# Performance work log

Measured on AMD Instinct MI355X. Metric: run time of the kernel, lower is better.

The kernel has to match this reference:

```python
import jax, jax.numpy as jnp
import numpy as np

NUM_HEADS = 32
EPS = 1e-5
NEG_INF = -1e9


def _ln(x, g, b):
    m = x.mean(-1, keepdims=True)
    v = ((x - m) ** 2).mean(-1, keepdims=True)
    return (x - m) / jnp.sqrt(v + EPS) * g + b


def setup_inputs() -> dict:
    key = jax.random.key(0)
    ks = jax.random.split(key, 20)
    N, B, D, E, F, L = 512, 2, 768, 256, 3072, 4
    inp = {
        'x': jax.random.normal(ks[0], (N, B, D), jnp.float32),
        'pos': jax.random.normal(ks[1], (B, N, 3), jnp.float32) * 5.0,
        'padding_mask': jnp.broadcast_to(jnp.arange(N)[None, :] >= N - 32, (B, N)),
        'outcell_index': jax.random.randint(ks[2], (B, E), 0, N),
        'expand_pos': jax.random.normal(ks[3], (B, E, 3), jnp.float32) * 5.0,
        'expand_mask': jnp.broadcast_to(jnp.arange(E)[None, :] >= E - 16, (B, E)),
        'vec_project_w': jax.random.normal(ks[4], (D, 3 * D), jnp.float32) * 0.02,
        'ln_x_g': jnp.ones((L, D), jnp.float32),
        'ln_x_b': jnp.zeros((L, D), jnp.float32),
        'ln_vec_g': jnp.ones((L, D), jnp.float32),
        'ln_vec_b': jnp.zeros((L, D), jnp.float32),
        'adaln_x_w': jax.random.normal(ks[5], (L, D, D), jnp.float32) * 0.02,
        'adaln_vecmlp_w': jax.random.normal(ks[6], (L, D, 2 * D), jnp.float32) * 0.02,
        'out_proj_w': jax.random.normal(ks[7], (L, D, D), jnp.float32) * 0.02,
        'vecmlp_norm_g': jnp.ones((L, D), jnp.float32),
        'vecmlp_norm_b': jnp.zeros((L, D), jnp.float32),
        'mlp_w1': jax.random.normal(ks[8], (L, D, F), jnp.float32) * 0.02,
        'mlp_w2': jax.random.normal(ks[9], (L, F, D), jnp.float32) * 0.02,
    }
    return inp


def reference(x, pos, padding_mask, outcell_index, expand_pos, expand_mask,
              vec_project_w, ln_x_g, ln_x_b, ln_vec_g, ln_vec_b,
              adaln_x_w, adaln_vecmlp_w, out_proj_w,
              vecmlp_norm_g, vecmlp_norm_b, mlp_w1, mlp_w2):
    x = jnp.swapaxes(x, 0, 1)  # [B,N,D]
    B, N, D = x.shape
    H = NUM_HEADS
    hd = D // H
    L = ln_x_g.shape[0]

    # --- PBC-expanded pairwise distance bias ---
    epf = jnp.concatenate([pos, expand_pos], axis=1)  # [B,S,3]
    S = epf.shape[1]
    delta = pos[:, :, None, :] - epf[:, None, :, :]   # [B,N,S,3]
    sq = (delta * delta).sum(-1)
    dist = jnp.where(sq > 0, jnp.sqrt(jnp.where(sq > 0, sq, 1.0)), 0.0)
    kpm_full = jnp.concatenate([padding_mask, expand_mask], axis=-1)  # [B,S]
    dist = jnp.where(padding_mask[:, :, None], 1e6, dist)
    dist = jnp.where(kpm_full[:, None, :], 1e6, dist)
    dist = 1.0 / (dist + 1.0)
    # additive attn mask (bias + key-padding -inf), broadcast over heads
    attn_mask = jnp.where(kpm_full[:, None, None, :], NEG_INF, dist[:, None, :, :])  # [B,1,N,S]

    vec = (jax.nn.silu(x) @ vec_project_w).reshape(B, N, 3, D)
    barange = jnp.arange(B)[:, None]
    scale = 1.0 / jnp.sqrt(jnp.float32(3 * hd))

    for l in range(L):
        rx, rv = x, vec
        xl = _ln(x, ln_x_g[l], ln_x_b[l])
        vl = _ln(vec, ln_vec_g[l], ln_vec_b[l])
        scale_x = jax.nn.silu(xl) @ adaln_x_w[l]        # [B,N,D]
        vmod = vl * scale_x[:, :, None, :]              # [B,N,3,D]
        # PBC gather-expanded K/V
        kv_exp = vmod[barange, outcell_index]           # [B,E,3,D]
        kv = jnp.concatenate([vmod, kv_exp], axis=1)    # [B,S,3,D]
        q = vmod.reshape(B, N, 3, H, hd).transpose(0, 3, 1, 2, 4).reshape(B, H, N, 3 * hd)
        k = kv.reshape(B, S, 3, H, hd).transpose(0, 3, 1, 2, 4).reshape(B, H, S, 3 * hd)
        v = k  # q=k=v in this block (same modulated vec)
        k = kv.reshape(B, S, 3, H, hd).transpose(0, 3, 1, 2, 4).reshape(B, H, S, 3 * hd)
        logits = jnp.einsum('bhnd,bhsd->bhns', q, k) * scale + attn_mask
        p = jax.nn.softmax(logits, axis=-1)
        o = jnp.einsum('bhns,bhsd->bhnd', p, v)          # [B,H,N,3hd]
        o = o.transpose(0, 2, 1, 3).reshape(B, N, H, 3, hd).transpose(0, 1, 3, 2, 4).reshape(B, N, 3, D)
        o = o @ out_proj_w[l]
        x = xl + rx
        vec = o + rv
        rx, rv = x, vec
        vm = _ln(vec, vecmlp_norm_g[l], vecmlp_norm_b[l])
        vm = jax.nn.silu(vm @ mlp_w1[l]) @ mlp_w2[l]     # [B,N,3,D]
        ss = jax.nn.silu(vm) @ adaln_vecmlp_w[l]         # [B,N,3,2D]
        sc, sh = jnp.split(ss, 2, axis=-1)
        x = x * sc.sum(-2) + sh.sum(-2) + rx
        vec = vm + rv
    return x, vec
```

## Files before the change

### kernel.cpp

```cpp
#include <hip/hip_runtime.h>

typedef __bf16 bf16_t;
typedef __bf16 bf8   __attribute__((ext_vector_type(8)));
typedef __bf16 bf4   __attribute__((ext_vector_type(4)));
typedef float  f32x4 __attribute__((ext_vector_type(4)));

__device__ __forceinline__ f32x4 mfma16(bf8 a, bf8 b, f32x4 c){
  return __builtin_amdgcn_mfma_f32_16x16x32_bf16(a, b, c, 0, 0, 0);
}
__device__ __forceinline__ float siluf_(float x){ return x / (1.f + __expf(-x)); }

__device__ __forceinline__ void async16(bf16_t* lds, const bf16_t* g){
  __builtin_amdgcn_global_load_lds(
      (const __attribute__((address_space(1))) unsigned int*)g,
      (__attribute__((address_space(3))) unsigned int*)lds, 16, 0, 0);
}

#define SCALE_QK 0.1178511302f

#define WT_VP   0ull
#define WT_AX   3538944ull
#define WT_AV   8257536ull
#define WT_OP   17694720ull
#define WT_M1   22413312ull
#define WT_M2   41287680ull
#define MASKB   60162048ull
#define SILUX   63307776ull
#define SILUXL  64880640ull
#define VLB     66453504ull
#define SCALEX  75890688ull
#define QKHB    79036416ull
#define KVTB    88473600ull
#define OBFB    97910784ull
#define VMLNB   102629376ull
#define H1B     107347968ull
#define SVM2B   126222336ull
#define SSB     130940928ull
#define MSOFF   10485760ull

struct TD { const float* s; bf16_t* d; int R, C, start, perz; };
struct TPack { TD t[6]; };

__global__ void transpose_all(TPack P)
{
  __shared__ bf16_t tile[64][66];
  const int bid = blockIdx.x;
  int k = 0;
  #pragma unroll
  for (int i = 1; i < 6; ++i) k = (bid >= P.t[i].start) ? i : k;
  const TD td = P.t[k];
  const int loc = bid - td.start;
  const int z = loc / td.perz, tl = loc - z*td.perz;
  const int nct = td.C >> 6;
  const int cx = tl % nct, ry = tl / nct;
  const size_t base = (size_t)z * td.R * td.C;
  const int r0 = ry*64, c0 = cx*64;
  const int t = threadIdx.x;
  #pragma unroll
  for (int j = 0; j < 4; ++j){
    int r = (t >> 4) + j*16;
    int cc = (t & 15) * 4;
    f32x4 v = *(const f32x4*)(td.s + base + (size_t)(r0 + r)*td.C + c0 + cc);
    #pragma unroll
    for (int e = 0; e < 4; ++e) tile[cc + e][r] = (bf16_t)v[e];
  }
  __syncthreads();
  #pragma unroll
  for (int j = 0; j < 2; ++j){
    int sid = j*256 + t;
    int c = sid >> 3, q = sid & 7;
    bf8 o = *(const bf8*)&tile[c][q*8];
    *(bf8*)(td.d + base + (size_t)(c0 + c)*td.R + r0 + q*8) = o;
  }
}

__global__ void mask_kernel(const float* __restrict__ pos, const float* __restrict__ epos,
                            bf16_t* __restrict__ wm)
{
  int i = blockIdx.x * 256 + threadIdx.x;
  int s = i % 768, t = i / 768;
  int n = t % 512, b = t / 512;
  bool kpm = (s < 512) ? (s >= 480) : (s >= 752);
  float o;
  if (kpm) o = 0.f;
  else {
    float d;
    if (n >= 480) d = 1e6f;
    else {
      const float* p = pos + (size_t)(b*512 + n)*3;
      const float* e = (s < 512) ? pos + (size_t)(b*512 + s)*3
                                 : epos + (size_t)(b*256 + (s-512))*3;
      float dx = p[0]-e[0], dy = p[1]-e[1], dz = p[2]-e[2];
      float sq = dx*dx + dy*dy + dz*dz;
      d = sq > 0.f ? sqrtf(sq) : 0.f;
    }
    o = __expf(1.f / (d + 1.f));
  }
  wm[i] = (bf16_t)o;
}

__global__ void xin_kernel(const float* __restrict__ xin, float* __restrict__ x,
                           bf16_t* __restrict__ sx)
{
  int i = blockIdx.x * 256 + threadIdx.x;
  int d = i % 768, t = i / 768;
  int n = t % 512, b = t / 512;
  float v = xin[((size_t)n*2 + b)*768 + d];
  x[i] = v;
  sx[i] = (bf16_t)siluf_(v);
}

__global__ __launch_bounds__(256,2) void ln_kernel(
    const float* __restrict__ in, const float* __restrict__ g, const float* __restrict__ bb,
    float* __restrict__ f32out, int addres, bf16_t* __restrict__ bfout, int dosilu)
{
  const int w = threadIdx.x >> 6, l = threadIdx.x & 63;
  const size_t r = (size_t)blockIdx.x * 4 + w;
  const float* p = in + r * 768;
  float v[12]; float s = 0.f;
  #pragma unroll
  for (int e = 0; e < 12; ++e){ v[e] = p[e*64 + l]; s += v[e]; }
  #pragma unroll
  for (int m = 1; m < 64; m <<= 1) s += __shfl_xor(s, m);
  float mean = s * (1.f/768.f);
  float q = 0.f;
  #pragma unroll
  for (int e = 0; e < 12; ++e){ float d = v[e] - mean; q += d*d; }
  #pragma unroll
  for (int m = 1; m < 64; m <<= 1) q += __shfl_xor(q, m);
  float rstd = rsqrtf(q * (1.f/768.f) + 1e-5f);
  #pragma unroll
  for (int e = 0; e < 12; ++e){
    int col = e*64 + l;
    float o = (v[e] - mean) * rstd * g[col] + bb[col];
    if (f32out) f32out[r*768 + col] = addres ? (o + v[e]) : o;
    if (bfout)  bfout[r*768 + col]  = (bf16_t)(dosilu ? siluf_(o) : o);
  }
}

__global__ __launch_bounds__(256,2) void pack2_kernel(
    const bf16_t* __restrict__ vl, const bf16_t* __restrict__ scx,
    const int* __restrict__ idx, bf16_t* __restrict__ qkh, bf16_t* __restrict__ kvt)
{
  __shared__ bf16_t tile[32*100];
  const int sb = blockIdx.x, bh = blockIdx.y;
  const int b = bh >> 5, h = bh & 31;
  const int tid = threadIdx.x;
  #pragma unroll
  for (int i = 0; i < 12; ++i){
    int e = i*256 + tid;
    int s_l = e / 96, col = e % 96;
    int s = sb*32 + s_l;
    float v = 0.f;
    if (col < 72){
      int n = (s < 512) ? s : idx[b*256 + (s - 512)];
      int c = col / 24, jj = col - c*24;
      int d = h*24 + jj;
      v = (float)vl[((size_t)(b*512 + n)*3 + c)*768 + d]
        * (float)scx[(size_t)(b*512 + n)*768 + d];
    }
    bf16_t bv = (bf16_t)v;
    qkh[((size_t)bh*768 + s)*96 + col] = bv;
    tile[s_l*100 + col] = bv;
  }
  __syncthreads();
  #pragma unroll
  for (int i = 0; i < 12; ++i){
    int f = i*256 + tid;
    int col = f >> 5, s_l = f & 31;
    kvt[((size_t)bh*96 + col)*768 + sb*32 + s_l] = tile[s_l*100 + col];
  }
}

__global__ __launch_bounds__(256,2) void attn_kernel(
    const bf16_t* __restrict__ qkh, const bf16_t* __restrict__ kvt,
    const bf16_t* __restrict__ wm, bf16_t* __restrict__ po, float* __restrict__ ms)
{
  __shared__ bf16_t Ks[64*128];
  __shared__ bf16_t Vs[96*72];
  __shared__ bf16_t Ps[64*72];
  const int g = blockIdx.x;
  const int qt = g >> 7, bhsz = g & 127;
  const int bh = bhsz & 63, sz = bhsz >> 6;
  const int b = bh >> 5;
  const int tid = threadIdx.x, w = tid >> 6, l = tid & 63;
  const int lg = l >> 4, lr = l & 15;
  const int sbase = sz * 384;
  const int qn0 = qt*64 + w*16 + lg*4;

  bf8 aq[3];
  {
    const bf16_t* qb = qkh + ((size_t)bh*768 + qt*64 + w*16 + lr)*96;
    #pragma unroll
    for (int ks = 0; ks < 3; ++ks) aq[ks] = *(const bf8*)(qb + ks*32 + lg*8);
  }

  int klds[3], vlds[3]; size_t kg[3], vg[3];
  #pragma unroll
  for (int it = 0; it < 3; ++it){
    int f = it*256 + tid;
    int r_ = f / 12, c_ = f % 12;
    klds[it] = r_*256 + ((c_*16) ^ ((r_ & 7) << 4));
    kg[it] = ((size_t)bh*768 + r_)*96 + c_*8;
    int vd = f >> 3, vc = (f & 7)*8;
    vlds[it] = vd*72 + vc;
    vg[it] = ((size_t)bh*96 + vd)*768 + vc;
  }

  f32x4 zf = {0.f,0.f,0.f,0.f};
  f32x4 accO[6];
  #pragma unroll
  for (int i = 0; i < 6; ++i) accO[i] = zf;
  float m_r[4], s_r[4];
  #pragma unroll
  for (int r = 0; r < 4; ++r){ m_r[r] = -1e30f; s_r[r] = 0.f; }

  bf8 kr[3], vr[3];
  #pragma unroll
  for (int it = 0; it < 3; ++it){
    kr[it] = *(const bf8*)(qkh + kg[it] + (size_t)sbase*96);
    vr[it] = *(const bf8*)(kvt + vg[it] + sbase);
  }
  #pragma unroll
  for (int it = 0; it < 3; ++it){
    *(bf8*)((char*)Ks + klds[it]) = kr[it];
    *(bf8*)&Vs[vlds[it]] = vr[it];
  }
  __syncthreads();

  const bf16_t* wrow = wm + (size_t)b*512*768;

  for (int t = 0; t < 6; ++t){
    const int s0 = sbase + t*64;
    if (t < 5){
      #pragma unroll
      for (int it = 0; it < 3; ++it){
        kr[it] = *(const bf8*)(qkh + kg[it] + (size_t)(s0 + 64)*96);
        vr[it] = *(const bf8*)(kvt + vg[it] + (s0 + 64));
      }
    }
    f32x4 sacc[4];
    __builtin_amdgcn_s_setprio(1);
    #pragma unroll
    for (int sf = 0; sf < 4; ++sf){
      sacc[sf] = zf;
      const int row = sf*16 + lr;
      #pragma unroll
      for (int ks = 0; ks < 3; ++ks){
        bf8 bg = *(const bf8*)((const char*)Ks + row*256 + ((ks*64 + lg*16) ^ ((row & 7) << 4)));
        sacc[sf] = mfma16(aq[ks], bg, sacc[sf]);
      }
    }
    __builtin_amdgcn_s_setprio(0);
    float tm[4];
    #pragma unroll
    for (int r = 0; r < 4; ++r)
      tm[r] = fmaxf(fmaxf(sacc[0][r], sacc[1][r]), fmaxf(sacc[2][r], sacc[3][r]));
    #pragma unroll
    for (int m = 1; m < 16; m <<= 1)
      #pragma unroll
      for (int r = 0; r < 4; ++r) tm[r] = fmaxf(tm[r], __shfl_xor(tm[r], m));
    float al[4], ps[4];
    #pragma unroll
    for (int r = 0; r < 4; ++r){
      float mn = fmaxf(m_r[r], tm[r]);
      al[r] = __expf((m_r[r] - mn)*SCALE_QK);
      m_r[r] = mn; ps[r] = 0.f;
    }
    #pragma unroll
    for (int sf = 0; sf < 4; ++sf)
      #pragma unroll
      for (int r = 0; r < 4; ++r){
        float p = __expf((sacc[sf][r] - m_r[r])*SCALE_QK)
                  * (float)wrow[(size_t)(qn0 + r)*768 + s0 + sf*16 + lr];
        ps[r] += p;
        Ps[(w*16 + lg*4 + r)*72 + sf*16 + lr] = (bf16_t)p;
      }
    #pragma unroll
    for (int m = 1; m < 16; m <<= 1)
      #pragma unroll
      for (int r = 0; r < 4; ++r) ps[r] += __shfl_xor(ps[r], m);
    #pragma unroll
    for (int r = 0; r < 4; ++r) s_r[r] = s_r[r]*al[r] + ps[r];
    #pragma unroll
    for (int df = 0; df < 6; ++df){
      f32x4 tt = accO[df];
      #pragma unroll
      for (int r = 0; r < 4; ++r) tt[r] *= al[r];
      accO[df] = tt;
    }
    __builtin_amdgcn_s_setprio(1);
    #pragma unroll
    for (int k2 = 0; k2 < 2; ++k2){
      bf8 pa = *(const bf8*)&Ps[(w*16 + lr)*72 + k2*32 + lg*8];
      #pragma unroll
      for (int df = 0; df < 6; ++df)
        accO[df] = mfma16(pa, *(const bf8*)&Vs[(df*16 + lr)*72 + k2*32 + lg*8], accO[df]);
    }
    __builtin_amdgcn_s_setprio(0);
    if (t < 5){
      __syncthreads();
      #pragma unroll
      for (int it = 0; it < 3; ++it){
        *(bf8*)((char*)Ks + klds[it]) = kr[it];
        *(bf8*)&Vs[vlds[it]] = vr[it];
      }
      __syncthreads();
    }
  }
  const size_t rbase = (size_t)(sz*64 + bh)*512;
  #pragma unroll
  for (int df = 0; df < 6; ++df){
    int dp = df*16 + lr;
    if (dp < 72){
      #pragma unroll
      for (int r = 0; r < 4; ++r)
        po[(rbase + qn0 + r)*80 + dp] = (bf16_t)accO[df][r];
    }
  }
  if (lr == 0){
    #pragma unroll
    for (int r = 0; r < 4; ++r){
      ms[(rbase + qn0 + r)*2]     = m_r[r];
      ms[(rbase + qn0 + r)*2 + 1] = s_r[r];
    }
  }
}

__global__ void attn_combine(const bf16_t* __restrict__ po, const float* __restrict__ ms,
                             bf16_t* __restrict__ obf)
{
  int t = blockIdx.x * 256 + threadIdx.x;
  int c = t % 12, row = t / 12;
  if (c >= 9) return;
  int bh = row >> 9, q = row & 511;
  int b = bh >> 5, h = bh & 31;
  float m1 = ms[(size_t)row*2],           s1 = ms[(size_t)row*2 + 1];
  float m2 = ms[(size_t)(32768 + row)*2], s2 = ms[(size_t)(32768 + row)*2 + 1];
  float m = fmaxf(m1, m2);
  float a1 = __expf((m1 - m)*SCALE_QK), a2 = __expf((m2 - m)*SCALE_QK);
  float rden = 1.f / (s1*a1 + s2*a2);
  bf8 o1 = *(const bf8*)(po + (size_t)row*80 + c*8);
  bf8 o2 = *(const bf8*)(po + (size_t)(32768 + row)*80 + c*8);
  bf8 o;
  #pragma unroll
  for (int r = 0; r < 8; ++r)
    o[r] = (bf16_t)(((float)o1[r]*a1 + (float)o2[r]*a2) * rden);
  int comp = c / 3, jj0 = (c % 3)*8;
  *(bf8*)(obf + ((size_t)(b*512 + q)*3 + comp)*768 + h*24 + jj0) = o;
}

template<int EPI>
__global__ __launch_bounds__(512,4) void gemm2(
    const bf16_t* __restrict__ A, const bf16_t* __restrict__ Bt,
    float* __restrict__ Cf, bf16_t* __restrict__ Cb,
    int M, int Nn, int K, int Ksub, int ntiles)
{
  __shared__ bf16_t As[128*64];
  __shared__ bf16_t Bs[128*64];
  const int tid = threadIdx.x;
  const int w = tid >> 6, l = tid & 63;
  const int lg = l >> 4, lr = l & 15;
  const int gb = blockIdx.x;
  const int sidx = gb >> 3, xcd = gb & 7;
  const int nt = sidx % ntiles;
  const int mt = xcd + (sidx / ntiles) * 8;
  const int wm = (w >> 2) * 64, wn = (w & 3) * 32;

  const int srow = w*8 + (l >> 3);
  const int scol = (((l & 7) ^ (l >> 3)) << 3);
  const bf16_t* Ab = A  + (size_t)(mt*128) * K;
  const bf16_t* Bb = Bt + (size_t)(nt*128) * K;
  const int kbeg = blockIdx.z * Ksub;

  f32x4 zf = {0.f,0.f,0.f,0.f};
  f32x4 acc[4][2];
  #pragma unroll
  for (int i = 0; i < 4; ++i)
    #pragma unroll
    for (int j = 0; j < 2; ++j) acc[i][j] = zf;

  int offA[4], offB[2];
  #pragma unroll
  for (int i = 0; i < 4; ++i){
    int row = wm + i*16 + lr;
    offA[i] = row*128 + ((lg*16) ^ ((row & 7) << 4));
  }
  #pragma unroll
  for (int j = 0; j < 2; ++j){
    int row = wn + j*16 + lr;
    offB[j] = row*128 + ((lg*16) ^ ((row & 7) << 4));
  }

  for (int k0 = kbeg; k0 < kbeg + Ksub; k0 += 64){
    __syncthreads();
    #pragma unroll
    for (int c = 0; c < 2; ++c){
      async16(&As[c*4096 + w*512], Ab + (size_t)(c*64 + srow)*K + k0 + scol);
      async16(&Bs[c*4096 + w*512], Bb + (size_t)(c*64 + srow)*K + k0 + scol);
    }
    __syncthreads();
    #pragma unroll
    for (int kk = 0; kk < 2; ++kk){
      bf8 af[4], bg[2];
      #pragma unroll
      for (int i = 0; i < 4; ++i)
        af[i] = *(const bf8*)((const char*)As + (offA[i] ^ (kk*64)));
      #pragma unroll
      for (int j = 0; j < 2; ++j)
        bg[j] = *(const bf8*)((const char*)Bs + (offB[j] ^ (kk*64)));
      #pragma unroll
      for (int i = 0; i < 4; ++i)
        #pragma unroll
        for (int j = 0; j < 2; ++j)
          acc[i][j] = mfma16(af[i], bg[j], acc[i][j]);
    }
  }

  const size_t zoff = (EPI == 4) ? (size_t)blockIdx.z * M * Nn : 0;
  #pragma unroll
  for (int i = 0; i < 4; ++i){
    int r0 = mt*128 + wm + i*16 + lg*4;
    #pragma unroll
    for (int j = 0; j < 2; ++j){
      int cc = nt*128 + wn + j*16 + lr;
      #pragma unroll
      for (int r = 0; r < 4; ++r){
        size_t off = (size_t)(r0 + r)*Nn + cc;
        float v = acc[i][j][r];
        if constexpr (EPI == 0)      Cf[off] = v;
        else if constexpr (EPI == 2) Cb[off] = (bf16_t)siluf_(v);
        else                         Cf[zoff + off] = v;
      }
    }
  }
}

__global__ void reduce4_bf(const float* __restrict__ p, bf16_t* __restrict__ out)
{
  int i = blockIdx.x * 256 + threadIdx.x;
  const f32x4* p4 = (const f32x4*)p;
  f32x4 a = p4[i], b = p4[i + 196608], c = p4[i + 393216], d = p4[i + 589824];
  bf4 o;
  #pragma unroll
  for (int r = 0; r < 4; ++r) o[r] = (bf16_t)(a[r] + b[r] + c[r] + d[r]);
  ((bf4*)out)[i] = o;
}

__global__ __launch_bounds__(256,2) void redop_ln(
    const float* __restrict__ p, float* __restrict__ vec,
    const float* __restrict__ g, const float* __restrict__ bb,
    bf16_t* __restrict__ vmln)
{
  const int w = threadIdx.x >> 6, l = threadIdx.x & 63;
  const size_t r = (size_t)blockIdx.x * 4 + w;
  float v[12]; float s = 0.f;
  #pragma unroll
  for (int e = 0; e < 12; ++e){
    size_t off = r*768 + e*64 + l;
    float t = vec[off] + p[off] + p[off + 2359296] + p[off + 4718592];
    vec[off] = t;
    v[e] = t; s += t;
  }
  #pragma unroll
  for (int m = 1; m < 64; m <<= 1) s += __shfl_xor(s, m);
  float mean = s * (1.f/768.f);
  float q = 0.f;
  #pragma unroll
  for (int e = 0; e < 12; ++e){ float d = v[e] - mean; q += d*d; }
  #pragma unroll
  for (int m = 1; m < 64; m <<= 1) q += __shfl_xor(q, m);
  float rstd = rsqrtf(q * (1.f/768.f) + 1e-5f);
  #pragma unroll
  for (int e = 0; e < 12; ++e){
    int col = e*64 + l;
    vmln[r*768 + col] = (bf16_t)((v[e] - mean) * rstd * g[col] + bb[col]);
  }
}

__global__ __launch_bounds__(256,2) void redmlp2_ln(
    const float* __restrict__ p, float* __restrict__ vec,
    bf16_t* __restrict__ svm2s,
    const float* __restrict__ g, const float* __restrict__ bb,
    bf16_t* __restrict__ vlb, int doln)
{
  const int w = threadIdx.x >> 6, l = threadIdx.x & 63;
  const size_t bn = (size_t)blockIdx.x * 4 + w;
  float ssum[12];
  #pragma unroll
  for (int e = 0; e < 12; ++e) ssum[e] = 0.f;
  for (int c = 0; c < 3; ++c){
    const size_t r = bn*3 + c;
    float v[12]; float s = 0.f;
    #pragma unroll
    for (int e = 0; e < 12; ++e){
      size_t off = r*768 + e*64 + l;
      float tm = p[off] + p[off + 2359296];
      float t = vec[off] + tm;
      vec[off] = t;
      v[e] = t; s += t;
      ssum[e] += siluf_(tm);
    }
    if (doln){
      #pragma unroll
      for (int m = 1; m < 64; m <<= 1) s += __shfl_xor(s, m);
      float mean = s * (1.f/768.f);
      float q = 0.f;
      #pragma unroll
      for (int e = 0; e < 12; ++e){ float d = v[e] - mean; q += d*d; }
      #pragma unroll
      for (int m = 1; m < 64; m <<= 1) q += __shfl_xor(q, m);
      float rstd = rsqrtf(q * (1.f/768.f) + 1e-5f);
      #pragma unroll
      for (int e = 0; e < 12; ++e){
        int col = e*64 + l;
        vlb[r*768 + col] = (bf16_t)((v[e] - mean) * rstd * g[col] + bb[col]);
      }
    }
  }
  #pragma unroll
  for (int e = 0; e < 12; ++e)
    svm2s[bn*768 + e*64 + l] = (bf16_t)ssum[e];
}

__global__ __launch_bounds__(256,2) void comb_ln(
    const float* __restrict__ p, float* __restrict__ x,
    const float* __restrict__ g, const float* __restrict__ bb,
    bf16_t* __restrict__ siluxl)
{
  const int w = threadIdx.x >> 6, l = threadIdx.x & 63;
  const size_t r = (size_t)blockIdx.x * 4 + w;
  const size_t base = r * 1536;
  float v[12]; float s = 0.f;
  #pragma unroll
  for (int e = 0; e < 12; ++e){
    int col = e*64 + l;
    float sc = p[base + col] + p[base + col + 1572864];
    float sh = p[base + 768 + col] + p[base + 768 + col + 1572864];
    float xv = x[r*768 + col]*(1.f + sc) + sh;
    v[e] = xv; s += xv;
  }
  #pragma unroll
  for (int m = 1; m < 64; m <<= 1) s += __shfl_xor(s, m);
  float mean = s * (1.f/768.f);
  float q = 0.f;
  #pragma unroll
  for (int e = 0; e < 12; ++e){ float d = v[e] - mean; q += d*d; }
  #pragma unroll
  for (int m = 1; m < 64; m <<= 1) q += __shfl_xor(q, m);
  float rstd = rsqrtf(q * (1.f/768.f) + 1e-5f);
  #pragma unroll
  for (int e = 0; e < 12; ++e){
    int col = e*64 + l;
    float xl = (v[e] - mean) * rstd * g[col] + bb[col];
    x[r*768 + col] = xl + v[e];
    siluxl[r*768 + col] = (bf16_t)siluf_(xl);
  }
}

__global__ void combine_kernel(const float* __restrict__ p, float* __restrict__ x)
{
  int i = blockIdx.x * 256 + threadIdx.x;
  size_t base = (size_t)(i / 768)*1536 + (i % 768);
  float sc = p[base] + p[base + 1572864];
  float sh = p[base + 768] + p[base + 768 + 1572864];
  x[i] = x[i]*(1.f + sc) + sh;
}

extern "C" void kernel_launch(void* const* d_in, const int* in_sizes, int n_in,
                              void* d_out, int out_size, void* d_ws, size_t ws_size,
                              hipStream_t stream)
{
  const float* x_in = (const float*)d_in[0];
  const float* pos  = (const float*)d_in[1];
  const int*   idx  = (const int*)d_in[3];
  const float* epos = (const float*)d_in[4];
  const float* vp_w = (const float*)d_in[6];
  const float* lxg  = (const float*)d_in[7];
  const float* lxb  = (const float*)d_in[8];
  const float* lvg  = (const float*)d_in[9];
  const float* lvb  = (const float*)d_in[10];
  const float* axw  = (const float*)d_in[11];
  const float* avw  = (const float*)d_in[12];
  const float* opw  = (const float*)d_in[13];
  const float* vng  = (const float*)d_in[14];
  const float* vnb  = (const float*)d_in[15];
  const float* w1   = (const float*)d_in[16];
  const float* w2   = (const float*)d_in[17];

  char* ws = (char*)d_ws;
  bf16_t* wt_vp = (bf16_t*)(ws + WT_VP);
  bf16_t* wt_ax = (bf16_t*)(ws + WT_AX);
  bf16_t* wt_av = (bf16_t*)(ws + WT_AV);
  bf16_t* wt_op = (bf16_t*)(ws + WT_OP);
  bf16_t* wt_m1 = (bf16_t*)(ws + WT_M1);
  bf16_t* wt_m2 = (bf16_t*)(ws + WT_M2);
  bf16_t* wmask = (bf16_t*)(ws + MASKB);
  bf16_t* silux = (bf16_t*)(ws + SILUX);
  bf16_t* siluxl= (bf16_t*)(ws + SILUXL);
  bf16_t* vlb   = (bf16_t*)(ws + VLB);
  bf16_t* scxb  = (bf16_t*)(ws + SCALEX);
  bf16_t* qkh   = (bf16_t*)(ws + QKHB);
  bf16_t* kvt   = (bf16_t*)(ws + KVTB);
  float*  partQ = (float*)(ws + QKHB);
  float*  partV = (float*)(ws + VLB);
  bf16_t* obf   = (bf16_t*)(ws + OBFB);
  bf16_t* vmln  = (bf16_t*)(ws + VMLNB);
  bf16_t* h1    = (bf16_t*)(ws + H1B);
  bf16_t* svm2s = (bf16_t*)(ws + SVM2B);
  bf16_t* pob   = (bf16_t*)(ws + SSB);
  float*  msb   = (float*)(ws + SSB + MSOFF);

  float* x   = (float*)d_out;
  float* vec = x + 786432;

  TPack P;
  P.t[0] = { vp_w, wt_vp, 768, 2304,    0,  432 };
  P.t[1] = { axw,  wt_ax, 768,  768,  432,  144 };
  P.t[2] = { avw,  wt_av, 768, 1536, 1008,  288 };
  P.t[3] = { opw,  wt_op, 768,  768, 2160,  144 };
  P.t[4] = { w1,   wt_m1, 768, 3072, 2736,  576 };
  P.t[5] = { w2,   wt_m2, 3072, 768, 5040,  576 };
  transpose_all<<<7344, 256, 0, stream>>>(P);

  mask_kernel<<<3072, 256, 0, stream>>>(pos, epos, wmask);
  xin_kernel<<<3072, 256, 0, stream>>>(x_in, x, silux);

  gemm2<0><<<dim3(8*18,1,1), 512, 0, stream>>>(silux, wt_vp, vec, nullptr,
                                               1024, 2304, 768, 768, 18);
  ln_kernel<<<256, 256, 0, stream>>>(x, lxg, lxb, x, 1, siluxl, 1);
  ln_kernel<<<768, 256, 0, stream>>>(vec, lvg, lvb, nullptr, 0, vlb, 0);

  for (int l = 0; l < 4; ++l){
    gemm2<4><<<dim3(8*6,1,4), 512, 0, stream>>>(siluxl, wt_ax + (size_t)l*768*768, partQ,
                                                nullptr, 1024, 768, 768, 192, 6);
    reduce4_bf<<<768, 256, 0, stream>>>(partQ, scxb);
    pack2_kernel<<<dim3(24, 64), 256, 0, stream>>>(vlb, scxb, idx, qkh, kvt);
    attn_kernel<<<1024, 256, 0, stream>>>(qkh, kvt, wmask, pob, msb);
    attn_combine<<<1536, 256, 0, stream>>>(pob, msb, obf);
    gemm2<4><<<dim3(24*6,1,3), 512, 0, stream>>>(obf, wt_op + (size_t)l*768*768, partV,
                                                 nullptr, 3072, 768, 768, 256, 6);
    redop_ln<<<768, 256, 0, stream>>>(partV, vec, vng + l*768, vnb + l*768, vmln);
    gemm2<2><<<dim3(24*24,1,1), 512, 0, stream>>>(vmln, wt_m1 + (size_t)l*3072*768, nullptr,
                                                  h1, 3072, 3072, 768, 768, 24);
    gemm2<4><<<dim3(24*6,1,2), 512, 0, stream>>>(h1, wt_m2 + (size_t)l*768*3072, partQ,
                                                 nullptr, 3072, 768, 3072, 1536, 6);
    redmlp2_ln<<<256, 256, 0, stream>>>(partQ, vec, svm2s,
                                        lvg + (l+1 < 4 ? (l+1)*768 : 0),
                                        lvb + (l+1 < 4 ? (l+1)*768 : 0),
                                        vlb, (l < 3) ? 1 : 0);
    gemm2<4><<<dim3(8*12,1,2), 512, 0, stream>>>(svm2s, wt_av + (size_t)l*1536*768, partQ,
                                                 nullptr, 1024, 1536, 768, 384, 12);
    if (l < 3)
      comb_ln<<<256, 256, 0, stream>>>(partQ, x, lxg + (l+1)*768, lxb + (l+1)*768, siluxl);
    else
      combine_kernel<<<3072, 256, 0, stream>>>(partQ, x);
  }
}
```

Baseline: 705.1 us.

## Drop attention split-KV combine pass and merge prologue kernels into one launch

The attention kernel now walks the full 768-key range in one block per (query tile, batch-head), normalises by the running sum and writes the final output layout directly, which removes the partial-output buffers and the separate combine kernel. The weight transpose, mask build and input copy are merged into one prologue launch, and the transpose now uses 64x128 tiles with a swizzled LDS layout and packed bf4 stores. This cuts four launches per forward and the partial-result traffic, but halves the attention grid (512 blocks), so there is less parallelism and a longer serial key loop per block.

After: 686.4 us. 1.03x faster.

```diff
diff --git a/kernel.cpp b/kernel.cpp
--- a/kernel.cpp
+++ b/kernel.cpp
@@ -35,79 +35,90 @@
 #define VMLNB   102629376ull
 #define H1B     107347968ull
 #define SVM2B   126222336ull
-#define SSB     130940928ull
-#define MSOFF   10485760ull
 
 struct TD { const float* s; bf16_t* d; int R, C, start, perz; };
 struct TPack { TD t[6]; };
 
-__global__ void transpose_all(TPack P)
-{
-  __shared__ bf16_t tile[64][66];
+#define NTRB 3672
+
+__global__ void prologue(TPack P,
+                         const float* __restrict__ pos, const float* __restrict__ epos,
+                         bf16_t* __restrict__ wm,
+                         const float* __restrict__ xin, float* __restrict__ x,
+                         bf16_t* __restrict__ sx)
+{
+  __shared__ bf16_t tile[128*72];
   const int bid = blockIdx.x;
+  const int t = threadIdx.x;
+  if (bid >= NTRB + 3072){
+    int i = (bid - NTRB - 3072) * 256 + t;
+    int d = i % 768, tt = i / 768;
+    int n = tt % 512, b = tt / 512;
+    float v = xin[((size_t)n*2 + b)*768 + d];
+    x[i] = v;
+    sx[i] = (bf16_t)siluf_(v);
+    return;
+  }
+  if (bid >= NTRB){
+    int i = (bid - NTRB) * 256 + t;
+    int s = i % 768, tt = i / 768;
+    int n = tt % 512, b = tt / 512;
+    bool kpm = (s < 512) ? (s >= 480) : (s >= 752);
+    float o;
+    if (kpm) o = 0.f;
+    else {
+      float d;
+      if (n >= 480) d = 1e6f;
+      else {
+        const float* p = pos + (size_t)(b*512 + n)*3;
+        const float* e = (s < 512) ? pos + (size_t)(b*512 + s)*3
+                                   : epos + (size_t)(b*256 + (s-512))*3;
+        float dx = p[0]-e[0], dy = p[1]-e[1], dz = p[2]-e[2];
+        float sq = dx*dx + dy*dy + dz*dz;
+        d = sq > 0.f ? sqrtf(sq) : 0.f;
+      }
+      o = __expf(1.f / (d + 1.f));
+    }
+    wm[i] = (bf16_t)o;
+    return;
+  }
   int k = 0;
   #pragma unroll
   for (int i = 1; i < 6; ++i) k = (bid >= P.t[i].start) ? i : k;
   const TD td = P.t[k];
   const int loc = bid - td.start;
   const int z = loc / td.perz, tl = loc - z*td.perz;
-  const int nct = td.C >> 6;
+  const int nct = td.C >> 7;
   const int cx = tl % nct, ry = tl / nct;
   const size_t base = (size_t)z * td.R * td.C;
-  const int r0 = ry*64, c0 = cx*64;
-  const int t = threadIdx.x;
-  #pragma unroll
-  for (int j = 0; j < 4; ++j){
-    int r = (t >> 4) + j*16;
-    int cc = (t & 15) * 4;
-    f32x4 v = *(const f32x4*)(td.s + base + (size_t)(r0 + r)*td.C + c0 + cc);
-    #pragma unroll
-    for (int e = 0; e < 4; ++e) tile[cc + e][r] = (bf16_t)v[e];
+  const int r0 = ry*64, c0 = cx*128;
+  #pragma unroll
+  for (int half = 0; half < 2; ++half){
+    int bb = half*256 + t;
+    int rb = bb >> 5, cb = bb & 31;
+    f32x4 v[4];
+    #pragma unroll
+    for (int i = 0; i < 4; ++i)
+      v[i] = *(const f32x4*)(td.s + base + (size_t)(r0 + rb*4 + i)*td.C + c0 + cb*4);
+    const int sw = (cb & 3) << 1;
+    const int rp = 4*(rb ^ sw);
+    #pragma unroll
+    for (int e = 0; e < 4; ++e){
+      bf4 pk;
+      #pragma unroll
+      for (int i = 0; i < 4; ++i) pk[i] = (bf16_t)v[i][e];
+      *(bf4*)&tile[(cb*4 + e)*72 + rp] = pk;
+    }
   }
   __syncthreads();
   #pragma unroll
-  for (int j = 0; j < 2; ++j){
-    int sid = j*256 + t;
+  for (int jj = 0; jj < 4; ++jj){
+    int sid = jj*256 + t;
     int c = sid >> 3, q = sid & 7;
-    bf8 o = *(const bf8*)&tile[c][q*8];
+    int qp = q ^ ((c >> 2) & 3);
+    bf8 o = *(const bf8*)&tile[c*72 + qp*8];
     *(bf8*)(td.d + base + (size_t)(c0 + c)*td.R + r0 + q*8) = o;
   }
-}
-
-__global__ void mask_kernel(const float* __restrict__ pos, const float* __restrict__ epos,
-                            bf16_t* __restrict__ wm)
-{
-  int i = blockIdx.x * 256 + threadIdx.x;
-  int s = i % 768, t = i / 768;
-  int n = t % 512, b = t / 512;
-  bool kpm = (s < 512) ? (s >= 480) : (s >= 752);
-  float o;
-  if (kpm) o = 0.f;
-  else {
-    float d;
-    if (n >= 480) d = 1e6f;
-    else {
-      const float* p = pos + (size_t)(b*512 + n)*3;
-      const float* e = (s < 512) ? pos + (size_t)(b*512 + s)*3
-                                 : epos + (size_t)(b*256 + (s-512))*3;
-      float dx = p[0]-e[0], dy = p[1]-e[1], dz = p[2]-e[2];
-      float sq = dx*dx + dy*dy + dz*dz;
-      d = sq > 0.f ? sqrtf(sq) : 0.f;
-    }
-    o = __expf(1.f / (d + 1.f));
-  }
-  wm[i] = (bf16_t)o;
-}
-
-__global__ void xin_kernel(const float* __restrict__ xin, float* __restrict__ x,
-                           bf16_t* __restrict__ sx)
-{
-  int i = blockIdx.x * 256 + threadIdx.x;
-  int d = i % 768, t = i / 768;
-  int n = t % 512, b = t / 512;
-  float v = xin[((size_t)n*2 + b)*768 + d];
-  x[i] = v;
-  sx[i] = (bf16_t)siluf_(v);
 }
 
 __global__ __launch_bounds__(256,2) void ln_kernel(
@@ -174,18 +185,16 @@
 
 __global__ __launch_bounds__(256,2) void attn_kernel(
     const bf16_t* __restrict__ qkh, const bf16_t* __restrict__ kvt,
-    const bf16_t* __restrict__ wm, bf16_t* __restrict__ po, float* __restrict__ ms)
+    const bf16_t* __restrict__ wm, bf16_t* __restrict__ obf)
 {
   __shared__ bf16_t Ks[64*128];
   __shared__ bf16_t Vs[96*72];
   __shared__ bf16_t Ps[64*72];
   const int g = blockIdx.x;
-  const int qt = g >> 7, bhsz = g & 127;
-  const int bh = bhsz & 63, sz = bhsz >> 6;
-  const int b = bh >> 5;
+  const int qt = g >> 6, bh = g & 63;
+  const int b = bh >> 5, h = bh & 31;
   const int tid = threadIdx.x, w = tid >> 6, l = tid & 63;
   const int lg = l >> 4, lr = l & 15;
-  const int sbase = sz * 384;
   const int qn0 = qt*64 + w*16 + lg*4;
 
   bf8 aq[3];
@@ -218,8 +227,8 @@
   bf8 kr[3], vr[3];
   #pragma unroll
   for (int it = 0; it < 3; ++it){
-    kr[it] = *(const bf8*)(qkh + kg[it] + (size_t)sbase*96);
-    vr[it] = *(const bf8*)(kvt + vg[it] + sbase);
+    kr[it] = *(const bf8*)(qkh + kg[it]);
+    vr[it] = *(const bf8*)(kvt + vg[it]);
   }
   #pragma unroll
   for (int it = 0; it < 3; ++it){
@@ -230,9 +239,9 @@
 
   const bf16_t* wrow = wm + (size_t)b*512*768;
 
-  for (int t = 0; t < 6; ++t){
-    const int s0 = sbase + t*64;
-    if (t < 5){
+  for (int t = 0; t < 12; ++t){
+    const int s0 = t*64;
+    if (t < 11){
       #pragma unroll
       for (int it = 0; it < 3; ++it){
         kr[it] = *(const bf8*)(qkh + kg[it] + (size_t)(s0 + 64)*96);
@@ -298,7 +307,7 @@
         accO[df] = mfma16(pa, *(const bf8*)&Vs[(df*16 + lr)*72 + k2*32 + lg*8], accO[df]);
     }
     __builtin_amdgcn_s_setprio(0);
-    if (t < 5){
+    if (t < 11){
       __syncthreads();
       #pragma unroll
       for (int it = 0; it < 3; ++it){
@@ -308,46 +317,19 @@
       __syncthreads();
     }
   }
-  const size_t rbase = (size_t)(sz*64 + bh)*512;
   #pragma unroll
   for (int df = 0; df < 6; ++df){
     int dp = df*16 + lr;
     if (dp < 72){
-      #pragma unroll
-      for (int r = 0; r < 4; ++r)
-        po[(rbase + qn0 + r)*80 + dp] = (bf16_t)accO[df][r];
-    }
-  }
-  if (lr == 0){
-    #pragma unroll
-    for (int r = 0; r < 4; ++r){
-      ms[(rbase + qn0 + r)*2]     = m_r[r];
-      ms[(rbase + qn0 + r)*2 + 1] = s_r[r];
-    }
-  }
-}
-
-__global__ void attn_combine(const bf16_t* __restrict__ po, const float* __restrict__ ms,
-                             bf16_t* __restrict__ obf)
-{
-  int t = blockIdx.x * 256 + threadIdx.x;
-  int c = t % 12, row = t / 12;
-  if (c >= 9) return;
-  int bh = row >> 9, q = row & 511;
-  int b = bh >> 5, h = bh & 31;
-  float m1 = ms[(size_t)row*2],           s1 = ms[(size_t)row*2 + 1];
-  float m2 = ms[(size_t)(32768 + row)*2], s2 = ms[(size_t)(32768 + row)*2 + 1];
-  float m = fmaxf(m1, m2);
-  float a1 = __expf((m1 - m)*SCALE_QK), a2 = __expf((m2 - m)*SCALE_QK);
-  float rden = 1.f / (s1*a1 + s2*a2);
-  bf8 o1 = *(const bf8*)(po + (size_t)row*80 + c*8);
-  bf8 o2 = *(const bf8*)(po + (size_t)(32768 + row)*80 + c*8);
-  bf8 o;
-  #pragma unroll
-  for (int r = 0; r < 8; ++r)
-    o[r] = (bf16_t)(((float)o1[r]*a1 + (float)o2[r]*a2) * rden);
-  int comp = c / 3, jj0 = (c % 3)*8;
-  *(bf8*)(obf + ((size_t)(b*512 + q)*3 + comp)*768 + h*24 + jj0) = o;
+      int c = dp / 24, jj = dp - c*24;
+      #pragma unroll
+      for (int r = 0; r < 4; ++r){
+        float v = accO[df][r] / s_r[r];
+        int qn = qn0 + r;
+        obf[((size_t)(b*512 + qn)*3 + c)*768 + h*24 + jj] = (bf16_t)v;
+      }
+    }
+  }
 }
 
 template<int EPI>
@@ -608,23 +590,18 @@
   bf16_t* vmln  = (bf16_t*)(ws + VMLNB);
   bf16_t* h1    = (bf16_t*)(ws + H1B);
   bf16_t* svm2s = (bf16_t*)(ws + SVM2B);
-  bf16_t* pob   = (bf16_t*)(ws + SSB);
-  float*  msb   = (float*)(ws + SSB + MSOFF);
 
   float* x   = (float*)d_out;
   float* vec = x + 786432;
 
   TPack P;
-  P.t[0] = { vp_w, wt_vp, 768, 2304,    0,  432 };
-  P.t[1] = { axw,  wt_ax, 768,  768,  432,  144 };
-  P.t[2] = { avw,  wt_av, 768, 1536, 1008,  288 };
-  P.t[3] = { opw,  wt_op, 768,  768, 2160,  144 };
-  P.t[4] = { w1,   wt_m1, 768, 3072, 2736,  576 };
-  P.t[5] = { w2,   wt_m2, 3072, 768, 5040,  576 };
-  transpose_all<<<7344, 256, 0, stream>>>(P);
-
-  mask_kernel<<<3072, 256, 0, stream>>>(pos, epos, wmask);
-  xin_kernel<<<3072, 256, 0, stream>>>(x_in, x, silux);
+  P.t[0] = { vp_w, wt_vp, 768, 2304,    0,  216 };
+  P.t[1] = { axw,  wt_ax, 768,  768,  216,   72 };
+  P.t[2] = { avw,  wt_av, 768, 1536,  504,  144 };
+  P.t[3] = { opw,  wt_op, 768,  768, 1080,   72 };
+  P.t[4] = { w1,   wt_m1, 768, 3072, 1368,  288 };
+  P.t[5] = { w2,   wt_m2, 3072, 768, 2520,  288 };
+  prologue<<<NTRB + 6144, 256, 0, stream>>>(P, pos, epos, wmask, x_in, x, silux);
 
   gemm2<0><<<dim3(8*18,1,1), 512, 0, stream>>>(silux, wt_vp, vec, nullptr,
                                                1024, 2304, 768, 768, 18);
@@ -636,8 +613,7 @@
                                                 nullptr, 1024, 768, 768, 192, 6);
     reduce4_bf<<<768, 256, 0, stream>>>(partQ, scxb);
     pack2_kernel<<<dim3(24, 64), 256, 0, stream>>>(vlb, scxb, idx, qkh, kvt);
-    attn_kernel<<<1024, 256, 0, stream>>>(qkh, kvt, wmask, pob, msb);
-    attn_combine<<<1536, 256, 0, stream>>>(pob, msb, obf);
+    attn_kernel<<<512, 256, 0, stream>>>(qkh, kvt, wmask, obf);
     gemm2<4><<<dim3(24*6,1,3), 512, 0, stream>>>(obf, wt_op + (size_t)l*768*768, partV,
                                                  nullptr, 3072, 768, 768, 256, 6);
     redop_ln<<<768, 256, 0, stream>>>(partV, vec, vng + l*768, vnb + l*768, vmln);
```
